# Performance work log

Hardware: AMD Instinct MI355X
Metric: run time of the kernel (lower is better)

## Reference

```python
import jax, jax.numpy as jnp
import numpy as np

V, D, H, DFF, L, B, S = 50257, 512, 8, 2048, 4, 2, 1024
MAXS = 1024
EPS = 1e-5


def _ln(x, g, b):
    m = x.mean(-1, keepdims=True)
    v = ((x - m) ** 2).mean(-1, keepdims=True)
    return (x - m) * jax.lax.rsqrt(v + EPS) * g + b


def setup_inputs() -> dict:
    key = jax.random.key(0)
    ks = jax.random.split(key, 20)
    n = lambda k, shape, s=0.02: jax.random.normal(k, shape, jnp.float32) * s
    return {
        "tokens": jax.random.randint(ks[0], (B, S), 0, V),
        "embedding": n(ks[1], (V, D)),
        "pos_embedding": n(ks[2], (1, MAXS, D)),
        # attention projections, torch Linear layout [out, in], stacked over layers
        "Wq": n(ks[3], (L, D, D), 0.03), "bq": jnp.zeros((L, D)),
        "Wk": n(ks[4], (L, D, D), 0.03), "bk": jnp.zeros((L, D)),
        "Wv": n(ks[5], (L, D, D), 0.03), "bv": jnp.zeros((L, D)),
        "Wo": n(ks[6], (L, D, D), 0.03), "bo": jnp.zeros((L, D)),
        "ln1_g": jnp.ones((L, D)), "ln1_b": jnp.zeros((L, D)),
        "W1": n(ks[7], (L, DFF, D), 0.03), "b1": jnp.zeros((L, DFF)),
        "W2": n(ks[8], (L, D, DFF), 0.03), "b2": jnp.zeros((L, D)),
        "ln2_g": jnp.ones((L, D)), "ln2_b": jnp.zeros((L, D)),
        "lnf_g": jnp.ones((D,)), "lnf_b": jnp.zeros((D,)),
        "Whead": n(ks[9], (V, D), 0.02), "bhead": jnp.zeros((V,)),
    }


def reference(tokens, embedding, pos_embedding, Wq, bq, Wk, bk, Wv, bv, Wo, bo,
              ln1_g, ln1_b, W1, b1, W2, b2, ln2_g, ln2_b, lnf_g, lnf_b,
              Whead, bhead):
    Bb, Ss = tokens.shape
    d_model = embedding.shape[1]
    dk = d_model // H
    x = embedding[tokens] + pos_embedding[:, :Ss, :]        # [B,S,D]
    causal = jnp.tril(jnp.ones((Ss, Ss), bool))             # [S,S]
    n_layers = Wq.shape[0]
    for l in range(n_layers):
        # pre-norm attention
        h = _ln(x, ln1_g[l], ln1_b[l])
        q = (h @ Wq[l].T + bq[l]).reshape(Bb, Ss, H, dk)
        k = (h @ Wk[l].T + bk[l]).reshape(Bb, Ss, H, dk)
        v = (h @ Wv[l].T + bv[l]).reshape(Bb, Ss, H, dk)
        scores = jnp.einsum('bqhd,bkhd->bhqk', q, k) / jnp.sqrt(jnp.float32(dk))
        scores = jnp.where(causal, scores, -jnp.inf)
        attn = jax.nn.softmax(scores, axis=-1)
        o = jnp.einsum('bhqk,bkhd->bqhd', attn, v).reshape(Bb, Ss, d_model)
        x = x + o @ Wo[l].T + bo[l]
        # pre-norm FFN (exact erf GELU, matching F.gelu default)
        h = _ln(x, ln2_g[l], ln2_b[l])
        x = x + jax.nn.gelu(h @ W1[l].T + b1[l], approximate=False) @ W2[l].T + b2[l]
    x = _ln(x, lnf_g, lnf_b)
    logits = x @ Whead.T + bhead                            # [B,S,V]
    return logits
```

## Files before the change

### kernel.cpp

```cpp
#include <hip/hip_runtime.h>
#include <hip/hip_bf16.h>
#include <math.h>

typedef __hip_bfloat16 bf16;
typedef __attribute__((ext_vector_type(8))) short bf16x8;
typedef __attribute__((ext_vector_type(4))) float f32x4;

#define SEQ    1024
#define DMODEL 512
#define NTOK   2048
#define VOCAB  50257
#define NDFF   2048

__device__ __forceinline__ void async_cp16(const bf16* g, bf16* s) {
  __builtin_amdgcn_global_load_lds((const __attribute__((address_space(1))) void*)g,
                                   (__attribute__((address_space(3))) void*)s, 16, 0, 0);
}

template<int MODE>
__global__ __launch_bounds__(256, 2) void gemm_nt(
    const bf16* A, long long sAb, long long sAh, int lda,
    const bf16* B, long long sBb, long long sBh, int ldb,
    const float* bias,
    void* Cptr, long long sCb, long long sCh, int ldc,
    const float* resid, int N, int K, int causal)
{
  if (causal && blockIdx.y > blockIdx.x) return;
  int z = blockIdx.z;
  A += (size_t)(z >> 3) * sAb + (size_t)(z & 7) * sAh;
  B += (size_t)(z >> 3) * sBb + (size_t)(z & 7) * sBh;
  size_t coff = (size_t)(z >> 3) * sCb + (size_t)(z & 7) * sCh;

  __shared__ bf16 smA[128 * 32];
  __shared__ bf16 smB[128 * 32];

  const int tid  = threadIdx.x;
  const int wave = tid >> 6, lane = tid & 63;
  const int m0 = blockIdx.x * 128, n0 = blockIdx.y * 128;

  f32x4 acc[4][4];
#pragma unroll
  for (int r = 0; r < 4; ++r)
#pragma unroll
    for (int c = 0; c < 4; ++c) acc[r][c] = (f32x4){0.f, 0.f, 0.f, 0.f};

  const int kc0 = (tid & 3) * 8;
  const int rA0 = m0 + (tid >> 2);
  const int rA1 = rA0 + 64;
  int rB0 = n0 + (tid >> 2);      if (rB0 > N - 1) rB0 = N - 1;
  int rB1 = n0 + 64 + (tid >> 2); if (rB1 > N - 1) rB1 = N - 1;
  const bf16* a0 = A + (size_t)rA0 * lda + kc0;
  const bf16* a1 = A + (size_t)rA1 * lda + kc0;
  const bf16* b0 = B + (size_t)rB0 * ldb + kc0;
  const bf16* b1 = B + (size_t)rB1 * ldb + kc0;
  bf16* sA0 = smA + wave * 512;
  bf16* sA1 = smA + 2048 + wave * 512;
  bf16* sB0 = smB + wave * 512;
  bf16* sB1 = smB + 2048 + wave * 512;

  const int fmA = (wave >> 1) * 64 + (lane & 15);
  const int fnB = (wave & 1) * 64 + (lane & 15);
  const int kq  = (lane >> 4) * 8;
  const short* sa = (const short*)smA;
  const short* sb = (const short*)smB;

  for (int k0 = 0; k0 < K; k0 += 32) {
    async_cp16(a0, sA0); async_cp16(a1, sA1);
    async_cp16(b0, sB0); async_cp16(b1, sB1);
    a0 += 32; a1 += 32; b0 += 32; b1 += 32;
    __syncthreads();
    bf16x8 af[4], bfr[4];
#pragma unroll
    for (int r = 0; r < 4; ++r) af[r]  = *(const bf16x8*)(sa + (fmA + r * 16) * 32 + kq);
#pragma unroll
    for (int c = 0; c < 4; ++c) bfr[c] = *(const bf16x8*)(sb + (fnB + c * 16) * 32 + kq);
#pragma unroll
    for (int r = 0; r < 4; ++r)
#pragma unroll
      for (int c = 0; c < 4; ++c)
        acc[r][c] = __builtin_amdgcn_mfma_f32_16x16x32_bf16(af[r], bfr[c], acc[r][c], 0, 0, 0);
    __syncthreads();
  }

  const int cm = m0 + (wave >> 1) * 64 + (lane >> 4) * 4;
  const int cn = n0 + (wave & 1) * 64 + (lane & 15);
#pragma unroll
  for (int c = 0; c < 4; ++c) {
    int gcol = cn + c * 16;
    if (gcol >= N) continue;
    float bv = bias ? bias[gcol] : 0.f;
#pragma unroll
    for (int r = 0; r < 4; ++r) {
#pragma unroll
      for (int i = 0; i < 4; ++i) {
        int grow = cm + r * 16 + i;
        float v = acc[r][c][i] + bv;
        size_t idx = coff + (size_t)grow * ldc + gcol;
        if (MODE == 0) ((float*)Cptr)[idx] = v;
        else if (MODE == 1) ((bf16*)Cptr)[idx] = __float2bfloat16(v);
        else if (MODE == 2) ((float*)Cptr)[idx] = resid[idx] + v;
        else {
          float gl = 0.5f * v * (1.f + erff(v * 0.70710678118654752f));
          ((bf16*)Cptr)[idx] = __float2bfloat16(gl);
        }
      }
    }
  }
}

__global__ __launch_bounds__(256) void ln_bf16(const float* __restrict__ x,
                                               const float* __restrict__ g,
                                               const float* __restrict__ b,
                                               bf16* __restrict__ out) {
  int row = blockIdx.x, tid = threadIdx.x;
  const float* xr = x + (size_t)row * DMODEL;
  float2 v = *(const float2*)(xr + tid * 2);
  float s = v.x + v.y, q = v.x * v.x + v.y * v.y;
#pragma unroll
  for (int o = 32; o; o >>= 1) { s += __shfl_down(s, o); q += __shfl_down(q, o); }
  __shared__ float ps[4], pq[4];
  int wave = tid >> 6, lane = tid & 63;
  if (!lane) { ps[wave] = s; pq[wave] = q; }
  __syncthreads();
  s = ps[0] + ps[1] + ps[2] + ps[3];
  q = pq[0] + pq[1] + pq[2] + pq[3];
  float mean = s * (1.f / DMODEL);
  float var  = q * (1.f / DMODEL) - mean * mean;
  float rstd = rsqrtf(var + 1e-5f);
  int d = tid * 2;
  out[(size_t)row * DMODEL + d]     = __float2bfloat16((v.x - mean) * rstd * g[d] + b[d]);
  out[(size_t)row * DMODEL + d + 1] = __float2bfloat16((v.y - mean) * rstd * g[d + 1] + b[d + 1]);
}

__global__ __launch_bounds__(256) void embed_k(const int* __restrict__ tok,
                                               const float* __restrict__ emb,
                                               const float* __restrict__ pos,
                                               float* __restrict__ x) {
  int t = blockIdx.x, tid = threadIdx.x;
  int s = t & (SEQ - 1);
  int id = tok[t];
  float2 e = *(const float2*)(emb + (size_t)id * DMODEL + tid * 2);
  float2 p = *(const float2*)(pos + (size_t)s * DMODEL + tid * 2);
  float2 o; o.x = e.x + p.x; o.y = e.y + p.y;
  *(float2*)(x + (size_t)t * DMODEL + tid * 2) = o;
}

__global__ __launch_bounds__(256) void softmax_causal(const float* __restrict__ s,
                                                      bf16* __restrict__ p) {
  int row = blockIdx.x;
  int i = row & (SEQ - 1);
  const float* sr = s + (size_t)row * SEQ;
  bf16* pr = p + (size_t)row * SEQ;
  int tid = threadIdx.x, wave = tid >> 6, lane = tid & 63;
  float v[4]; float m = -3.4e38f;
#pragma unroll
  for (int t = 0; t < 4; ++t) {
    int j = tid + t * 256;
    float x = (j <= i) ? sr[j] : -3.4e38f;
    v[t] = x; m = fmaxf(m, x);
  }
#pragma unroll
  for (int o = 32; o; o >>= 1) m = fmaxf(m, __shfl_down(m, o));
  __shared__ float red[4];
  if (!lane) red[wave] = m;
  __syncthreads();
  m = fmaxf(fmaxf(red[0], red[1]), fmaxf(red[2], red[3]));
  __syncthreads();
  float e[4]; float sum = 0.f;
#pragma unroll
  for (int t = 0; t < 4; ++t) {
    int j = tid + t * 256;
    float x = (j <= i) ? expf((v[t] - m) * 0.125f) : 0.f;
    e[t] = x; sum += x;
  }
#pragma unroll
  for (int o = 32; o; o >>= 1) sum += __shfl_down(sum, o);
  if (!lane) red[wave] = sum;
  __syncthreads();
  float r = 1.f / (red[0] + red[1] + red[2] + red[3]);
#pragma unroll
  for (int t = 0; t < 4; ++t) pr[tid + t * 256] = __float2bfloat16(e[t] * r);
}

__global__ __launch_bounds__(256) void transpose_v(const bf16* __restrict__ v,
                                                   bf16* __restrict__ vT) {
  int bh = blockIdx.x;
  int b = bh >> 3, h = bh & 7;
  int jt = blockIdx.y * 64;
  const bf16* vb = v + (size_t)b * SEQ * DMODEL + h * 64;
  bf16* vo = vT + (size_t)bh * 64 * SEQ + jt;
#pragma unroll
  for (int it = 0; it < 16; ++it) {
    int e = it * 256 + threadIdx.x;
    int j = e & 63, d = e >> 6;
    vo[(size_t)d * SEQ + j] = vb[(size_t)(jt + j) * DMODEL + d];
  }
}

__global__ __launch_bounds__(256) void cvt_bf16(const float* __restrict__ in,
                                                bf16* __restrict__ out, int n) {
  int i = (blockIdx.x * 256 + threadIdx.x) * 4;
  if (i + 3 < n) {
    float4 v = *(const float4*)(in + i);
    out[i]     = __float2bfloat16(v.x);
    out[i + 1] = __float2bfloat16(v.y);
    out[i + 2] = __float2bfloat16(v.z);
    out[i + 3] = __float2bfloat16(v.w);
  } else {
    for (; i < n; ++i) out[i] = __float2bfloat16(in[i]);
  }
}

extern "C" void kernel_launch(void* const* d_in, const int* in_sizes, int n_in,
                              void* d_out, int out_size, void* d_ws, size_t ws_size,
                              hipStream_t stream) {
  const int*   tokens = (const int*)d_in[0];
  const float* emb    = (const float*)d_in[1];
  const float* pos    = (const float*)d_in[2];
  const float* Wq = (const float*)d_in[3];  const float* bq = (const float*)d_in[4];
  const float* Wk = (const float*)d_in[5];  const float* bk = (const float*)d_in[6];
  const float* Wv = (const float*)d_in[7];  const float* bv = (const float*)d_in[8];
  const float* Wo = (const float*)d_in[9];  const float* bo = (const float*)d_in[10];
  const float* ln1g = (const float*)d_in[11]; const float* ln1b = (const float*)d_in[12];
  const float* W1 = (const float*)d_in[13]; const float* b1 = (const float*)d_in[14];
  const float* W2 = (const float*)d_in[15]; const float* b2 = (const float*)d_in[16];
  const float* ln2g = (const float*)d_in[17]; const float* ln2b = (const float*)d_in[18];
  const float* lnfg = (const float*)d_in[19]; const float* lnfb = (const float*)d_in[20];
  const float* Whead = (const float*)d_in[21]; const float* bhead = (const float*)d_in[22];
  float* out = (float*)d_out;

  char* w = (char*)d_ws;
  auto carve = [&](size_t bytes) -> char* {
    char* p = w; w += (bytes + 255) & ~(size_t)255; return p;
  };
  bf16* wWq = (bf16*)carve((size_t)4 * 512 * 512 * 2);
  bf16* wWk = (bf16*)carve((size_t)4 * 512 * 512 * 2);
  bf16* wWv = (bf16*)carve((size_t)4 * 512 * 512 * 2);
  bf16* wWo = (bf16*)carve((size_t)4 * 512 * 512 * 2);
  bf16* wW1 = (bf16*)carve((size_t)4 * NDFF * 512 * 2);
  bf16* wW2 = (bf16*)carve((size_t)4 * NDFF * 512 * 2);
  bf16* wWh = (bf16*)carve((size_t)VOCAB * 512 * 2);
  float* xbuf = (float*)carve((size_t)NTOK * DMODEL * 4);
  bf16* hb  = (bf16*)carve((size_t)NTOK * DMODEL * 2);
  bf16* qb  = (bf16*)carve((size_t)NTOK * DMODEL * 2);
  bf16* kb  = (bf16*)carve((size_t)NTOK * DMODEL * 2);
  bf16* vb  = (bf16*)carve((size_t)NTOK * DMODEL * 2);
  bf16* vTb = (bf16*)carve((size_t)16 * 64 * SEQ * 2);
  bf16* ob  = (bf16*)carve((size_t)NTOK * DMODEL * 2);
  float* scores = (float*)carve((size_t)16 * SEQ * SEQ * 4);
  bf16* pb  = (bf16*)carve((size_t)16 * SEQ * SEQ * 2);
  bf16* h1b = (bf16*)carve((size_t)NTOK * NDFF * 2);
  (void)ws_size; (void)n_in; (void)in_sizes; (void)out_size;

  auto cvt = [&](const float* src, bf16* dst, int n) {
    cvt_bf16<<<(n / 4 + 255) / 256, 256, 0, stream>>>(src, dst, n);
  };
  cvt(Wq, wWq, 4 * 512 * 512);
  cvt(Wk, wWk, 4 * 512 * 512);
  cvt(Wv, wWv, 4 * 512 * 512);
  cvt(Wo, wWo, 4 * 512 * 512);
  cvt(W1, wW1, 4 * NDFF * 512);
  cvt(W2, wW2, 4 * NDFF * 512);
  cvt(Whead, wWh, VOCAB * 512);

  embed_k<<<NTOK, 256, 0, stream>>>(tokens, emb, pos, xbuf);

  const dim3 g16x4(16, 4, 1);
  for (int l = 0; l < 4; ++l) {
    const bf16* wq = wWq + (size_t)l * 512 * 512;
    const bf16* wk = wWk + (size_t)l * 512 * 512;
    const bf16* wv = wWv + (size_t)l * 512 * 512;
    const bf16* wo = wWo + (size_t)l * 512 * 512;
    const bf16* w1 = wW1 + (size_t)l * NDFF * 512;
    const bf16* w2 = wW2 + (size_t)l * NDFF * 512;

    ln_bf16<<<NTOK, 256, 0, stream>>>(xbuf, ln1g + l * 512, ln1b + l * 512, hb);
    gemm_nt<1><<<g16x4, 256, 0, stream>>>(hb, 0, 0, 512, wq, 0, 0, 512, bq + l * 512,
                                          qb, 0, 0, 512, nullptr, 512, 512, 0);
    gemm_nt<1><<<g16x4, 256, 0, stream>>>(hb, 0, 0, 512, wk, 0, 0, 512, bk + l * 512,
                                          kb, 0, 0, 512, nullptr, 512, 512, 0);
    gemm_nt<1><<<g16x4, 256, 0, stream>>>(hb, 0, 0, 512, wv, 0, 0, 512, bv + l * 512,
                                          vb, 0, 0, 512, nullptr, 512, 512, 0);
    transpose_v<<<dim3(16, 16), 256, 0, stream>>>(vb, vTb);
    gemm_nt<0><<<dim3(8, 8, 16), 256, 0, stream>>>(
        qb, 524288, 64, 512, kb, 524288, 64, 512, nullptr,
        scores, 8388608, 1048576, 1024, nullptr, 1024, 64, 1);
    softmax_causal<<<16 * SEQ, 256, 0, stream>>>(scores, pb);
    gemm_nt<1><<<dim3(8, 1, 16), 256, 0, stream>>>(
        pb, 8388608, 1048576, 1024, vTb, 524288, 65536, 1024, nullptr,
        ob, 524288, 64, 512, nullptr, 64, 1024, 0);
    gemm_nt<2><<<g16x4, 256, 0, stream>>>(ob, 0, 0, 512, wo, 0, 0, 512, bo + l * 512,
                                          xbuf, 0, 0, 512, xbuf, 512, 512, 0);
    ln_bf16<<<NTOK, 256, 0, stream>>>(xbuf, ln2g + l * 512, ln2b + l * 512, hb);
    gemm_nt<3><<<dim3(16, 16, 1), 256, 0, stream>>>(hb, 0, 0, 512, w1, 0, 0, 512,
                                                    b1 + l * NDFF, h1b, 0, 0, NDFF,
                                                    nullptr, NDFF, 512, 0);
    gemm_nt<2><<<g16x4, 256, 0, stream>>>(h1b, 0, 0, NDFF, w2, 0, 0, NDFF, b2 + l * 512,
                                          xbuf, 0, 0, 512, xbuf, 512, NDFF, 0);
  }

  ln_bf16<<<NTOK, 256, 0, stream>>>(xbuf, lnfg, lnfb, hb);
  gemm_nt<0><<<dim3(16, 393, 1), 256, 0, stream>>>(hb, 0, 0, 512, wWh, 0, 0, 512, bhead,
                                                   out, 0, 0, VOCAB, nullptr, VOCAB, 512, 0);
}
```

Baseline: 1.689 ms.

## Replace materialized attention with fused flash attention and merge QKV projections

Replaces the QK^T GEMM, full-size fp32 score buffer, causal softmax kernel and PV GEMM with a single flash-attention kernel. Each wave handles a 16-row query tile with online softmax, skips fully masked KV tiles, and keeps P in LDS for the second MFMA. The three Q/K/V projections are fused into one GEMM over a concatenated weight and bias. This removes heavy intermediate memory traffic and several launches. In exchange, each wave does small tiles without cross-wave KV reuse, reloading K/V from global memory.

```diff
diff --git a/kernel.cpp b/kernel.cpp
--- a/kernel.cpp
+++ b/kernel.cpp
@@ -108,6 +108,126 @@
   }
 }
 
+__global__ __launch_bounds__(256) void flash_attn(const bf16* __restrict__ qkv,
+                                                  const bf16* __restrict__ vT,
+                                                  bf16* __restrict__ ob) {
+  const int wave = threadIdx.x >> 6, lane = threadIdx.x & 63;
+  const int g  = blockIdx.x * 4 + wave;
+  const int bh = g >> 6;
+  const int t6 = g & 63;
+  const int qt = (t6 & 1) ? (63 - (t6 >> 1)) : (t6 >> 1);
+  const int b = bh >> 3, h = bh & 7;
+  const int ln15 = lane & 15, hi = lane >> 4;
+  const int qg0 = qt * 16;
+  const int nkv = (qt >> 2) + 1;
+
+  __shared__ short smP[4][16 * 72];
+  short* Pw = smP[wave];
+
+  const bf16* qbase = qkv + (size_t)(b * SEQ + qg0 + ln15) * 1536 + h * 64 + hi * 8;
+  bf16x8 qf[2];
+  qf[0] = *(const bf16x8*)(qbase);
+  qf[1] = *(const bf16x8*)(qbase + 32);
+
+  const bf16* kbase = qkv + (size_t)(b * SEQ) * 1536 + 512 + h * 64
+                      + (size_t)ln15 * 1536 + hi * 8;
+  const bf16* vbase = vT + (size_t)bh * 64 * SEQ + (size_t)ln15 * SEQ + hi * 8;
+
+  float m[4], l[4];
+  f32x4 acco[4];
+#pragma unroll
+  for (int i = 0; i < 4; ++i) { m[i] = -3.4e38f; l[i] = 0.f; }
+#pragma unroll
+  for (int nf = 0; nf < 4; ++nf) acco[nf] = (f32x4){0.f, 0.f, 0.f, 0.f};
+
+  for (int jt = 0; jt < nkv; ++jt) {
+    const int kv0 = jt * 64;
+    bf16x8 kf[4][2];
+#pragma unroll
+    for (int cf = 0; cf < 4; ++cf) {
+      const bf16* kr = kbase + (size_t)(kv0 + cf * 16) * 1536;
+      kf[cf][0] = *(const bf16x8*)(kr);
+      kf[cf][1] = *(const bf16x8*)(kr + 32);
+    }
+    bf16x8 vf[4][2];
+#pragma unroll
+    for (int nf = 0; nf < 4; ++nf) {
+      const bf16* vr = vbase + (size_t)(nf * 16) * SEQ + kv0;
+      vf[nf][0] = *(const bf16x8*)(vr);
+      vf[nf][1] = *(const bf16x8*)(vr + 32);
+    }
+    f32x4 accs[4];
+#pragma unroll
+    for (int cf = 0; cf < 4; ++cf) {
+      accs[cf] = (f32x4){0.f, 0.f, 0.f, 0.f};
+      accs[cf] = __builtin_amdgcn_mfma_f32_16x16x32_bf16(qf[0], kf[cf][0], accs[cf], 0, 0, 0);
+      accs[cf] = __builtin_amdgcn_mfma_f32_16x16x32_bf16(qf[1], kf[cf][1], accs[cf], 0, 0, 0);
+    }
+    if (jt == nkv - 1) {
+#pragma unroll
+      for (int cf = 0; cf < 4; ++cf)
+#pragma unroll
+        for (int i = 0; i < 4; ++i)
+          if (kv0 + cf * 16 + ln15 > qg0 + hi * 4 + i) accs[cf][i] = -3.4e38f;
+    }
+    float mn[4], f[4];
+#pragma unroll
+    for (int i = 0; i < 4; ++i) {
+      float mm = fmaxf(fmaxf(accs[0][i], accs[1][i]), fmaxf(accs[2][i], accs[3][i]));
+#pragma unroll
+      for (int o = 1; o < 16; o <<= 1) mm = fmaxf(mm, __shfl_xor(mm, o));
+      mn[i] = fmaxf(m[i], mm);
+      f[i] = expf((m[i] - mn[i]) * 0.125f);
+      m[i] = mn[i];
+    }
+    float rs[4] = {0.f, 0.f, 0.f, 0.f};
+#pragma unroll
+    for (int cf = 0; cf < 4; ++cf)
+#pragma unroll
+      for (int i = 0; i < 4; ++i) {
+        float p = expf((accs[cf][i] - mn[i]) * 0.125f);
+        accs[cf][i] = p;
+        rs[i] += p;
+      }
+#pragma unroll
+    for (int i = 0; i < 4; ++i) {
+#pragma unroll
+      for (int o = 1; o < 16; o <<= 1) rs[i] += __shfl_xor(rs[i], o);
+      l[i] = l[i] * f[i] + rs[i];
+    }
+    asm volatile("" ::: "memory");
+#pragma unroll
+    for (int cf = 0; cf < 4; ++cf)
+#pragma unroll
+      for (int i = 0; i < 4; ++i) {
+        union { bf16 b; short s; } u;
+        u.b = __float2bfloat16(accs[cf][i]);
+        Pw[(hi * 4 + i) * 72 + cf * 16 + ln15] = u.s;
+      }
+    asm volatile("" ::: "memory");
+#pragma unroll
+    for (int nf = 0; nf < 4; ++nf)
+#pragma unroll
+      for (int i = 0; i < 4; ++i) acco[nf][i] *= f[i];
+    bf16x8 pf[2];
+    pf[0] = *(const bf16x8*)(Pw + ln15 * 72 + hi * 8);
+    pf[1] = *(const bf16x8*)(Pw + ln15 * 72 + 32 + hi * 8);
+#pragma unroll
+    for (int nf = 0; nf < 4; ++nf) {
+      acco[nf] = __builtin_amdgcn_mfma_f32_16x16x32_bf16(pf[0], vf[nf][0], acco[nf], 0, 0, 0);
+      acco[nf] = __builtin_amdgcn_mfma_f32_16x16x32_bf16(pf[1], vf[nf][1], acco[nf], 0, 0, 0);
+    }
+  }
+  bf16* orow = ob + (size_t)(b * SEQ + qg0 + hi * 4) * DMODEL + h * 64 + ln15;
+#pragma unroll
+  for (int i = 0; i < 4; ++i) {
+    float r = 1.f / l[i];
+#pragma unroll
+    for (int nf = 0; nf < 4; ++nf)
+      orow[(size_t)i * DMODEL + nf * 16] = __float2bfloat16(acco[nf][i] * r);
+  }
+}
+
 __global__ __launch_bounds__(256) void ln_bf16(const float* __restrict__ x,
                                                const float* __restrict__ g,
                                                const float* __restrict__ b,
@@ -145,55 +265,18 @@
   *(float2*)(x + (size_t)t * DMODEL + tid * 2) = o;
 }
 
-__global__ __launch_bounds__(256) void softmax_causal(const float* __restrict__ s,
-                                                      bf16* __restrict__ p) {
-  int row = blockIdx.x;
-  int i = row & (SEQ - 1);
-  const float* sr = s + (size_t)row * SEQ;
-  bf16* pr = p + (size_t)row * SEQ;
-  int tid = threadIdx.x, wave = tid >> 6, lane = tid & 63;
-  float v[4]; float m = -3.4e38f;
-#pragma unroll
-  for (int t = 0; t < 4; ++t) {
-    int j = tid + t * 256;
-    float x = (j <= i) ? sr[j] : -3.4e38f;
-    v[t] = x; m = fmaxf(m, x);
-  }
-#pragma unroll
-  for (int o = 32; o; o >>= 1) m = fmaxf(m, __shfl_down(m, o));
-  __shared__ float red[4];
-  if (!lane) red[wave] = m;
-  __syncthreads();
-  m = fmaxf(fmaxf(red[0], red[1]), fmaxf(red[2], red[3]));
-  __syncthreads();
-  float e[4]; float sum = 0.f;
-#pragma unroll
-  for (int t = 0; t < 4; ++t) {
-    int j = tid + t * 256;
-    float x = (j <= i) ? expf((v[t] - m) * 0.125f) : 0.f;
-    e[t] = x; sum += x;
-  }
-#pragma unroll
-  for (int o = 32; o; o >>= 1) sum += __shfl_down(sum, o);
-  if (!lane) red[wave] = sum;
-  __syncthreads();
-  float r = 1.f / (red[0] + red[1] + red[2] + red[3]);
-#pragma unroll
-  for (int t = 0; t < 4; ++t) pr[tid + t * 256] = __float2bfloat16(e[t] * r);
-}
-
-__global__ __launch_bounds__(256) void transpose_v(const bf16* __restrict__ v,
+__global__ __launch_bounds__(256) void transpose_v(const bf16* __restrict__ qkv,
                                                    bf16* __restrict__ vT) {
   int bh = blockIdx.x;
   int b = bh >> 3, h = bh & 7;
   int jt = blockIdx.y * 64;
-  const bf16* vb = v + (size_t)b * SEQ * DMODEL + h * 64;
+  const bf16* vb = qkv + (size_t)b * SEQ * 1536 + 1024 + h * 64;
   bf16* vo = vT + (size_t)bh * 64 * SEQ + jt;
 #pragma unroll
   for (int it = 0; it < 16; ++it) {
     int e = it * 256 + threadIdx.x;
     int j = e & 63, d = e >> 6;
-    vo[(size_t)d * SEQ + j] = vb[(size_t)(jt + j) * DMODEL + d];
+    vo[(size_t)d * SEQ + j] = vb[(size_t)(jt + j) * 1536 + d];
   }
 }
 
@@ -209,6 +292,30 @@
   } else {
     for (; i < n; ++i) out[i] = __float2bfloat16(in[i]);
   }
+}
+
+__global__ __launch_bounds__(256) void cvt_qkv(const float* __restrict__ Wq,
+                                               const float* __restrict__ Wk,
+                                               const float* __restrict__ Wv,
+                                               bf16* __restrict__ dst) {
+  int l = blockIdx.y, seg = blockIdx.z;
+  const float* src = (seg == 0 ? Wq : seg == 1 ? Wk : Wv) + (size_t)l * 262144;
+  bf16* d = dst + (size_t)l * 786432 + (size_t)seg * 262144;
+  int i = (blockIdx.x * 256 + threadIdx.x) * 4;
+  float4 v = *(const float4*)(src + i);
+  d[i]     = __float2bfloat16(v.x);
+  d[i + 1] = __float2bfloat16(v.y);
+  d[i + 2] = __float2bfloat16(v.z);
+  d[i + 3] = __float2bfloat16(v.w);
+}
+
+__global__ __launch_bounds__(512) void bias_qkv(const float* __restrict__ bq,
+                                                const float* __restrict__ bk,
+                                                const float* __restrict__ bv,
+                                                float* __restrict__ out) {
+  int l = blockIdx.x, seg = blockIdx.y, d = threadIdx.x;
+  const float* src = (seg == 0 ? bq : seg == 1 ? bk : bv);
+  out[(size_t)l * 1536 + seg * 512 + d] = src[(size_t)l * 512 + d];
 }
 
 extern "C" void kernel_launch(void* const* d_in, const int* in_sizes, int n_in,
@@ -233,31 +340,25 @@
   auto carve = [&](size_t bytes) -> char* {
     char* p = w; w += (bytes + 255) & ~(size_t)255; return p;
   };
-  bf16* wWq = (bf16*)carve((size_t)4 * 512 * 512 * 2);
-  bf16* wWk = (bf16*)carve((size_t)4 * 512 * 512 * 2);
-  bf16* wWv = (bf16*)carve((size_t)4 * 512 * 512 * 2);
-  bf16* wWo = (bf16*)carve((size_t)4 * 512 * 512 * 2);
-  bf16* wW1 = (bf16*)carve((size_t)4 * NDFF * 512 * 2);
-  bf16* wW2 = (bf16*)carve((size_t)4 * NDFF * 512 * 2);
-  bf16* wWh = (bf16*)carve((size_t)VOCAB * 512 * 2);
+  bf16*  wQKV = (bf16*)carve((size_t)4 * 1536 * 512 * 2);
+  bf16*  wWo  = (bf16*)carve((size_t)4 * 512 * 512 * 2);
+  bf16*  wW1  = (bf16*)carve((size_t)4 * NDFF * 512 * 2);
+  bf16*  wW2  = (bf16*)carve((size_t)4 * NDFF * 512 * 2);
+  bf16*  wWh  = (bf16*)carve((size_t)VOCAB * 512 * 2);
+  float* bQKV = (float*)carve((size_t)4 * 1536 * 4);
   float* xbuf = (float*)carve((size_t)NTOK * DMODEL * 4);
-  bf16* hb  = (bf16*)carve((size_t)NTOK * DMODEL * 2);
-  bf16* qb  = (bf16*)carve((size_t)NTOK * DMODEL * 2);
-  bf16* kb  = (bf16*)carve((size_t)NTOK * DMODEL * 2);
-  bf16* vb  = (bf16*)carve((size_t)NTOK * DMODEL * 2);
-  bf16* vTb = (bf16*)carve((size_t)16 * 64 * SEQ * 2);
-  bf16* ob  = (bf16*)carve((size_t)NTOK * DMODEL * 2);
-  float* scores = (float*)carve((size_t)16 * SEQ * SEQ * 4);
-  bf16* pb  = (bf16*)carve((size_t)16 * SEQ * SEQ * 2);
-  bf16* h1b = (bf16*)carve((size_t)NTOK * NDFF * 2);
+  bf16*  hb   = (bf16*)carve((size_t)NTOK * DMODEL * 2);
+  bf16*  qkvb = (bf16*)carve((size_t)NTOK * 1536 * 2);
+  bf16*  vTb  = (bf16*)carve((size_t)16 * 64 * SEQ * 2);
+  bf16*  ob   = (bf16*)carve((size_t)NTOK * DMODEL * 2);
+  bf16*  h1b  = (bf16*)carve((size_t)NTOK * NDFF * 2);
   (void)ws_size; (void)n_in; (void)in_sizes; (void)out_size;
 
   auto cvt = [&](const float* src, bf16* dst, int n) {
     cvt_bf16<<<(n / 4 + 255) / 256, 256, 0, stream>>>(src, dst, n);
   };
-  cvt(Wq, wWq, 4 * 512 * 512);
-  cvt(Wk, wWk, 4 * 512 * 512);
-  cvt(Wv, wWv, 4 * 512 * 512);
+  cvt_qkv<<<dim3(256, 4, 3), 256, 0, stream>>>(Wq, Wk, Wv, wQKV);
+  bias_qkv<<<dim3(4, 3), 512, 0, stream>>>(bq, bk, bv, bQKV);
   cvt(Wo, wWo, 4 * 512 * 512);
   cvt(W1, wW1, 4 * NDFF * 512);
   cvt(W2, wW2, 4 * NDFF * 512);
@@ -267,28 +368,17 @@
 
   const dim3 g16x4(16, 4, 1);
   for (int l = 0; l < 4; ++l) {
-    const bf16* wq = wWq + (size_t)l * 512 * 512;
-    const bf16* wk = wWk + (size_t)l * 512 * 512;
-    const bf16* wv = wWv + (size_t)l * 512 * 512;
+    const bf16* wqkv = wQKV + (size_t)l * 1536 * 512;
     const bf16* wo = wWo + (size_t)l * 512 * 512;
     const bf16* w1 = wW1 + (size_t)l * NDFF * 512;
     const bf16* w2 = wW2 + (size_t)l * NDFF * 512;
 
     ln_bf16<<<NTOK, 256, 0, stream>>>(xbuf, ln1g + l * 512, ln1b + l * 512, hb);
-    gemm_nt<1><<<g16x4, 256, 0, stream>>>(hb, 0, 0, 512, wq, 0, 0, 512, bq + l * 512,
-                                          qb, 0, 0, 512, nullptr, 512, 512, 0);
-    gemm_nt<1><<<g16x4, 256, 0, stream>>>(hb, 0, 0, 512, wk, 0, 0, 512, bk + l * 512,
-                                          kb, 0, 0, 512, nullptr, 512, 512, 0);
-    gemm_nt<1><<<g16x4, 256, 0, stream>>>(hb, 0, 0, 512, wv, 0, 0, 512, bv + l * 512,
-                                          vb, 0, 0, 512, nullptr, 512, 512, 0);
-    transpose_v<<<dim3(16, 16), 256, 0, stream>>>(vb, vTb);
-    gemm_nt<0><<<dim3(8, 8, 16), 256, 0, stream>>>(
-        qb, 524288, 64, 512, kb, 524288, 64, 512, nullptr,
-        scores, 8388608, 1048576, 1024, nullptr, 1024, 64, 1);
-    softmax_causal<<<16 * SEQ, 256, 0, stream>>>(scores, pb);
-    gemm_nt<1><<<dim3(8, 1, 16), 256, 0, stream>>>(
-        pb, 8388608, 1048576, 1024, vTb, 524288, 65536, 1024, nullptr,
-        ob, 524288, 64, 512, nullptr, 64, 1024, 0);
+    gemm_nt<1><<<dim3(16, 12, 1), 256, 0, stream>>>(
+        hb, 0, 0, 512, wqkv, 0, 0, 512, bQKV + l * 1536,
+        qkvb, 0, 0, 1536, nullptr, 1536, 512, 0);
+    transpose_v<<<dim3(16, 16), 256, 0, stream>>>(qkvb, vTb);
+    flash_attn<<<256, 256, 0, stream>>>(qkvb, vTb, ob);
     gemm_nt<2><<<g16x4, 256, 0, stream>>>(ob, 0, 0, 512, wo, 0, 0, 512, bo + l * 512,
                                           xbuf, 0, 0, 512, xbuf, 512, 512, 0);
     ln_bf16<<<NTOK, 256, 0, stream>>>(xbuf, ln2g + l * 512, ln2b + l * 512, hb);
```

New measurement: 1.452 ms. -14.0%, faster.
